# Performance work log

Hardware: AMD Instinct MI355X
Metric: run time of the kernel (lower is better)

Reference implementation:

```python
import jax, jax.numpy as jnp
import numpy as np

N, D_IN, D_OUT, E, TOPK = 2048, 2048, 2048, 8, 2


def setup_inputs() -> dict:
    key = jax.random.key(0)
    k1, k2, k3, k4 = jax.random.split(key, 4)
    inputs = jax.random.normal(k1, (N, D_IN), dtype=jnp.float32)
    weight = jax.random.normal(k2, (E, D_OUT, D_IN), dtype=jnp.float32) * (1.0 / np.sqrt(D_IN))
    gates = jax.random.uniform(k3, (N, TOPK), dtype=jnp.float32)
    gates = gates / jnp.sum(gates, axis=-1, keepdims=True)
    # random routing: expert id for each of the N*TOPK (token, slot) pairs
    expert_of = jax.random.randint(k4, (N * TOPK,), 0, E, dtype=jnp.int32)
    order = jnp.argsort(expert_of)  # positions sorted by expert id
    sorted_expert_idxs = expert_of[order].astype(jnp.int32)
    sorted_scattered_idxs = order.astype(jnp.int32)
    counts = jnp.bincount(expert_of, length=E)
    expert_offsets = jnp.cumsum(counts).astype(jnp.int32)
    padded_block_idxs = jnp.zeros((1,), dtype=jnp.int32)  # kernel blocking artifact, no math effect
    return {
        "inputs": inputs,
        "weight": weight,
        "k": TOPK,
        "sorted_expert_idxs": sorted_expert_idxs,
        "sorted_scattered_idxs": sorted_scattered_idxs,
        "padded_block_idxs": padded_block_idxs,
        "expert_offsets": expert_offsets,
        "gates": gates,
    }


def reference(inputs, weight, k, sorted_expert_idxs, sorted_scattered_idxs,
              padded_block_idxs, expert_offsets, gates):
    # inputs: [N, d_in]; weight: [E, d_out, d_in] (module permutes to [E, d_in, d_out])
    n_tok, d_in = inputs.shape
    n_e, d_out, _ = weight.shape
    nk = sorted_expert_idxs.shape[0]
    # invert the sort: expert id per flat (token, slot) position
    expert_of = jnp.zeros((nk,), dtype=sorted_expert_idxs.dtype).at[sorted_scattered_idxs].set(sorted_expert_idxs)
    x_flat = inputs[jnp.arange(nk) // k]  # [N*k, d_in] (fan-out of k per token)
    # grouped GEMM: y_flat[j] = x_flat[j] @ weight[expert_of[j]].T
    y_flat = jnp.zeros((nk, d_out), dtype=inputs.dtype)
    for e in range(n_e):  # loop over fixed small expert count (structural)
        mask = (expert_of == e)[:, None]
        y_flat = y_flat + jnp.where(mask, x_flat, 0.0) @ weight[e].T
    # gating combine: bmm(gates[:, None, :], y.view(N, k, d_out))
    out = jnp.einsum('nk,nkd->nd', gates, y_flat.reshape(n_tok, k, d_out))
    return out
```

## Files before the change

kernel.cpp:

```cpp
#include <hip/hip_runtime.h>
#include <hip/hip_bf16.h>

#define DIN   2048
#define DOUT  2048
#define NTOK  2048
#define NE    8
#define TOPK  2
#define NK    (NTOK*TOPK)
#define BM    256
#define BN    128
#define BK    32
#define KSPLIT 2
#define KLOC  (DIN/KSPLIT)
#define NKT   (KLOC/BK)
#define MAXMT (NK/BM + NE)
#define NTN   (DOUT/BN)
#define NBLK  (MAXMT*NTN*KSPLIT)

#define WEL (NE*DOUT*DIN)
#define XEL (NTOK*DIN)

typedef unsigned short u16;
typedef __attribute__((ext_vector_type(8))) short bf16x8;
typedef __attribute__((ext_vector_type(4))) float f32x4;

__device__ __forceinline__ unsigned pack2rn(float a, float b) {
    union { float f; unsigned u; } x, y; x.f = a; y.f = b;
    return __builtin_amdgcn_perm(y.u + 0x8000u, x.u + 0x8000u, 0x07060302u);
}

__device__ __forceinline__ void gl_lds16(const void* g, void* l) {
    __builtin_amdgcn_global_load_lds(
        (const __attribute__((address_space(1))) void*)g,
        (__attribute__((address_space(3)))       void*)l, 16, 0, 0);
}

__global__ __launch_bounds__(256) void cvt_x(
    const float* __restrict__ x, u16* __restrict__ xbf)
{
    const size_t nch = (size_t)XEL / 8;
    for (size_t c = (size_t)blockIdx.x * blockDim.x + threadIdx.x; c < nch;
         c += (size_t)gridDim.x * blockDim.x) {
        size_t off = c * 8;
        float4 f0 = *(const float4*)(x + off);
        float4 f1 = *(const float4*)(x + off + 4);
        uint4 pk;
        pk.x = pack2rn(f0.x, f0.y); pk.y = pack2rn(f0.z, f0.w);
        pk.z = pack2rn(f1.x, f1.y); pk.w = pack2rn(f1.z, f1.w);
        *(uint4*)(xbf + off) = pk;
    }
}

__global__ __launch_bounds__(512, 4) void moe_gemm_wf2(
    const u16*   __restrict__ xb,
    const float* __restrict__ wf,
    const int*   __restrict__ sorted_scattered_idxs,
    const int*   __restrict__ expert_offsets,
    const float* __restrict__ gates,
    float*       __restrict__ out)
{
    __shared__ u16 As[2][BM * BK];
    __shared__ u16 Bs[2][BN * BK];
    __shared__ int   s_tok[BM];
    __shared__ float s_gate[BM];

    const int bid = blockIdx.x;
    const int swz = (bid & 7) * (NBLK / 8) + (bid >> 3);
    const int n0  = (swz & (NTN - 1)) * BN;
    const int ksl = (swz >> 4) & (KSPLIT - 1);
    const int mt  = swz >> 5;

    int e = -1, m0 = 0, cnt = 0;
    {
        int acc0 = 0, prev = 0;
        for (int i = 0; i < NE; ++i) {
            int end = expert_offsets[i];
            int c = end - prev;
            int t = (c + BM - 1) / BM;
            if (mt < acc0 + t) {
                e = i; m0 = prev + (mt - acc0) * BM;
                cnt = end - m0; if (cnt > BM) cnt = BM;
                break;
            }
            acc0 += t; prev = end;
        }
    }
    if (e < 0) return;

    const int tid = threadIdx.x;
    if (tid < BM) {
        int idx = (tid < cnt) ? (m0 + tid) : m0;
        int p = sorted_scattered_idxs[idx];
        s_tok[tid]  = p;
        s_gate[tid] = gates[p];
    }
    __syncthreads();

    const int wid = tid >> 6, lane = tid & 63;
    const int kbase = ksl * KLOC;

    const int arow0 = wid * 16 + (lane >> 2);
    const int cga   = (lane & 3) ^ ((lane >> 3) & 3);
    const u16* aS0 = xb + (size_t)(s_tok[arow0] >> 1) * DIN + kbase + cga * 8;
    const u16* aS1 = xb + (size_t)(s_tok[arow0 + 128] >> 1) * DIN + kbase + cga * 8;
    const int adst0 = (wid * 16) * BK;
    const int adst1 = (128 + wid * 16) * BK;

    const int brow = tid >> 2;
    const int bch  = tid & 3;
    const int bcg  = bch ^ ((brow >> 1) & 3);
    const float* bF = wf + (size_t)e * DOUT * DIN + (size_t)(n0 + brow) * DIN + kbase + bch * 8;
    const int bwr = brow * BK + bcg * 8;

    const int wr = wid >> 2, wc = wid & 3;
    const int lr = lane & 15, g = lane >> 4;
    const int xch = (g ^ ((lr >> 1) & 3)) * 8;
    int aoff[8], boff[2];
    #pragma unroll
    for (int mi = 0; mi < 8; ++mi) aoff[mi] = (wr * 128 + mi * 16 + lr) * BK + xch;
    #pragma unroll
    for (int n = 0; n < 2; ++n)    boff[n]  = (wc * 32 + n * 16 + lr) * BK + xch;

    f32x4 acc[8][2];
    #pragma unroll
    for (int mi = 0; mi < 8; ++mi)
        #pragma unroll
        for (int n = 0; n < 2; ++n) acc[mi][n] = (f32x4)0.0f;

    float4 pb0, pb1;

#define STGA(buf, t)                                                          \
    {                                                                         \
        const int ko = (t) * BK;                                              \
        gl_lds16(aS0 + ko, &As[buf][adst0]);                                  \
        gl_lds16(aS1 + ko, &As[buf][adst1]);                                  \
    }

#define BGLB(t)                                                               \
    {                                                                         \
        const int ko = (t) * BK;                                              \
        pb0 = *(const float4*)(bF + ko);                                      \
        pb1 = *(const float4*)(bF + ko + 4);                                  \
    }

#define BPACK(buf)                                                            \
    {                                                                         \
        uint4 w;                                                              \
        w.x = pack2rn(pb0.x, pb0.y); w.y = pack2rn(pb0.z, pb0.w);             \
        w.z = pack2rn(pb1.x, pb1.y); w.w = pack2rn(pb1.z, pb1.w);             \
        *(uint4*)(&Bs[buf][bwr]) = w;                                         \
    }

#define BODY(b)                                                               \
    {                                                                         \
        bf16x8 bfv[2], af[4], ag[4];                                          \
        bfv[0] = *(const bf16x8*)(&Bs[b][boff[0]]);                           \
        bfv[1] = *(const bf16x8*)(&Bs[b][boff[1]]);                           \
        _Pragma("unroll")                                                     \
        for (int mi = 0; mi < 4; ++mi)                                        \
            af[mi] = *(const bf16x8*)(&As[b][aoff[mi]]);                      \
        __builtin_amdgcn_s_setprio(1);                                        \
        _Pragma("unroll")                                                     \
        for (int mi = 0; mi < 4; ++mi) {                                      \
            acc[mi][0] = __builtin_amdgcn_mfma_f32_16x16x32_bf16(             \
                af[mi], bfv[0], acc[mi][0], 0, 0, 0);                         \
            acc[mi][1] = __builtin_amdgcn_mfma_f32_16x16x32_bf16(             \
                af[mi], bfv[1], acc[mi][1], 0, 0, 0);                         \
        }                                                                     \
        _Pragma("unroll")                                                     \
        for (int mi = 0; mi < 4; ++mi)                                        \
            ag[mi] = *(const bf16x8*)(&As[b][aoff[mi + 4]]);                  \
        _Pragma("unroll")                                                     \
        for (int mi = 0; mi < 4; ++mi) {                                      \
            acc[mi+4][0] = __builtin_amdgcn_mfma_f32_16x16x32_bf16(           \
                ag[mi], bfv[0], acc[mi+4][0], 0, 0, 0);                       \
            acc[mi+4][1] = __builtin_amdgcn_mfma_f32_16x16x32_bf16(           \
                ag[mi], bfv[1], acc[mi+4][1], 0, 0, 0);                       \
        }                                                                     \
        __builtin_amdgcn_s_setprio(0);                                        \
        __builtin_amdgcn_s_barrier();                                        \
    }

    BGLB(0);
    STGA(0, 0);
    asm volatile("s_waitcnt vmcnt(0)" ::: "memory");
    __builtin_amdgcn_sched_barrier(0);
    BPACK(0);
    STGA(1, 1);
    BGLB(1);

    #pragma unroll 2
    for (int t = 0; t < NKT; ++t) {
        asm volatile("s_waitcnt lgkmcnt(0)" ::: "memory");
        __builtin_amdgcn_s_barrier();
        BODY(t & 1);
        asm volatile("s_waitcnt vmcnt(0)" ::: "memory");
        __builtin_amdgcn_sched_barrier(0);
        if (t + 1 < NKT) BPACK((t + 1) & 1);
        if (t + 2 < NKT) { STGA(t & 1, t + 2); BGLB(t + 2); }
    }

#undef STGA
#undef BGLB
#undef BPACK
#undef BODY

    #pragma unroll
    for (int mi = 0; mi < 8; ++mi) {
        #pragma unroll
        for (int r = 0; r < 4; ++r) {
            int lrow = wr * 128 + mi * 16 + g * 4 + r;
            if (lrow < cnt) {
                int   p  = s_tok[lrow];
                float gf = s_gate[lrow];
                float* orow = out + (size_t)(p >> 1) * DOUT + n0 + wc * 32;
                #pragma unroll
                for (int n = 0; n < 2; ++n)
                    atomicAdd(orow + n * 16 + lr, gf * acc[mi][n][r]);
            }
        }
    }
}

#define FBM 128
#define FBK 64
__global__ __launch_bounds__(256, 3) void moe_gemm_fused(
    const float* __restrict__ inputs, const float* __restrict__ weight,
    const int* __restrict__ sorted_scattered_idxs, const int* __restrict__ expert_offsets,
    const float* __restrict__ gates, float* __restrict__ out)
{
    __shared__ u16 As[FBM * FBK];
    __shared__ u16 Bs[FBM * FBK];
    __shared__ int   s_tok[FBM];
    __shared__ float s_gate[FBM];

    const int mt = blockIdx.y;
    const int n0 = blockIdx.x * FBM;
    int e = -1, m0 = 0, cnt = 0;
    {
        int acc = 0, prev = 0;
        for (int i = 0; i < NE; ++i) {
            int end = expert_offsets[i];
            int c = end - prev;
            int t = (c + FBM - 1) / FBM;
            if (mt < acc + t) {
                e = i; m0 = prev + (mt - acc) * FBM;
                cnt = end - m0; if (cnt > FBM) cnt = FBM;
                break;
            }
            acc += t; prev = end;
        }
    }
    if (e < 0) return;

    const int tid = threadIdx.x;
    if (tid < FBM) {
        int idx = (tid < cnt) ? (m0 + tid) : m0;
        int p = sorted_scattered_idxs[idx];
        s_tok[tid]  = p;
        s_gate[tid] = gates[p];
    }
    __syncthreads();

    const int ch  = tid & 7;
    const int r0  = tid >> 3;
    const int sch = ch ^ (r0 & 7);
    const float* wbase = weight + (size_t)e * DOUT * DIN;
    const float* ap[4]; const float* bp[4];
    #pragma unroll
    for (int i = 0; i < 4; ++i) {
        int r = r0 + 32 * i;
        ap[i] = inputs + (size_t)(s_tok[r] >> 1) * DIN + ch * 8;
        bp[i] = wbase + (size_t)(n0 + r) * DIN + ch * 8;
    }
    u16* aw = &As[r0 * FBK + sch * 8];
    u16* bw = &Bs[r0 * FBK + sch * 8];

    const int wid = tid >> 6, lane = tid & 63;
    const int wm = (wid >> 1) * 64, wn = (wid & 1) * 64;
    const int g  = lane >> 4, lr = lane & 15;

    f32x4 acc[4][4];
    #pragma unroll
    for (int i = 0; i < 4; ++i)
        #pragma unroll
        for (int j = 0; j < 4; ++j) acc[i][j] = (f32x4)0.0f;

    float4 pa[4][2], pb[4][2];
    #pragma unroll
    for (int i = 0; i < 4; ++i) {
        pa[i][0] = *(const float4*)(ap[i] + 0); pa[i][1] = *(const float4*)(ap[i] + 4);
        pb[i][0] = *(const float4*)(bp[i] + 0); pb[i][1] = *(const float4*)(bp[i] + 4);
    }
    for (int kt = 0; kt < DIN / FBK; ++kt) {
        __syncthreads();
        #pragma unroll
        for (int i = 0; i < 4; ++i) {
            uint4 va, vb;
            va.x = pack2rn(pa[i][0].x, pa[i][0].y); va.y = pack2rn(pa[i][0].z, pa[i][0].w);
            va.z = pack2rn(pa[i][1].x, pa[i][1].y); va.w = pack2rn(pa[i][1].z, pa[i][1].w);
            *(uint4*)(aw + i * 32 * FBK) = va;
            vb.x = pack2rn(pb[i][0].x, pb[i][0].y); vb.y = pack2rn(pb[i][0].z, pb[i][0].w);
            vb.z = pack2rn(pb[i][1].x, pb[i][1].y); vb.w = pack2rn(pb[i][1].z, pb[i][1].w);
            *(uint4*)(bw + i * 32 * FBK) = vb;
        }
        __syncthreads();
        if (kt + 1 < DIN / FBK) {
            const int kof = (kt + 1) * FBK;
            #pragma unroll
            for (int i = 0; i < 4; ++i) {
                pa[i][0] = *(const float4*)(ap[i] + kof); pa[i][1] = *(const float4*)(ap[i] + kof + 4);
                pb[i][0] = *(const float4*)(bp[i] + kof); pb[i][1] = *(const float4*)(bp[i] + kof + 4);
            }
        }
        #pragma unroll
        for (int ks = 0; ks < 2; ++ks) {
            bf16x8 a[4], b[4];
            #pragma unroll
            for (int i = 0; i < 4; ++i) {
                int ra = wm + i * 16 + lr; int ca = (ks * 4 + g) ^ (ra & 7);
                a[i] = *(const bf16x8*)(&As[ra * FBK + ca * 8]);
                int rb = wn + i * 16 + lr; int cb = (ks * 4 + g) ^ (rb & 7);
                b[i] = *(const bf16x8*)(&Bs[rb * FBK + cb * 8]);
            }
            #pragma unroll
            for (int i = 0; i < 4; ++i)
                #pragma unroll
                for (int j = 0; j < 4; ++j)
                    acc[i][j] = __builtin_amdgcn_mfma_f32_16x16x32_bf16(a[i], b[j], acc[i][j], 0, 0, 0);
        }
    }
    #pragma unroll
    for (int i = 0; i < 4; ++i) {
        #pragma unroll
        for (int j2 = 0; j2 < 4; ++j2) {
            int lrow = wm + i * 16 + g * 4 + j2;
            if (lrow < cnt) {
                int   p  = s_tok[lrow];
                float gf = s_gate[lrow];
                float* orow = out + (size_t)(p >> 1) * DOUT + n0 + wn;
                #pragma unroll
                for (int nf = 0; nf < 4; ++nf)
                    atomicAdd(orow + nf * 16 + lr, gf * acc[i][nf][j2]);
            }
        }
    }
}

extern "C" void kernel_launch(void* const* d_in, const int* in_sizes, int n_in,
                              void* d_out, int out_size, void* d_ws, size_t ws_size,
                              hipStream_t stream) {
    const float* inputs  = (const float*)d_in[0];
    const float* weight  = (const float*)d_in[1];
    const int*   ssi     = (const int*)d_in[4];
    const int*   eoff    = (const int*)d_in[6];
    const float* gates   = (const float*)d_in[7];
    float* out = (float*)d_out;

    hipMemsetAsync(out, 0, (size_t)out_size * sizeof(float), stream);

    const size_t need = (size_t)XEL * sizeof(u16);
    if (ws_size >= need) {
        u16* xbf = (u16*)d_ws;
        cvt_x<<<1024, 256, 0, stream>>>(inputs, xbf);
        moe_gemm_wf2<<<NBLK, 512, 0, stream>>>(xbf, weight, ssi, eoff, gates, out);
    } else {
        dim3 grid(DOUT / FBM, NK / FBM + NE);
        moe_gemm_fused<<<grid, 256, 0, stream>>>(inputs, weight, ssi, eoff, gates, out);
    }
}
```

Baseline: 113.1 us.

## Pre-convert weights to bf16 and stream both operands via direct-to-LDS loads

Expands the conversion kernel to also turn the fp32 expert weights into bf16 in the workspace. The GEMM then loads both A and B tiles with global_load_lds, dropping the register staging and in-loop packing of fp32 weights, and uses a vmcnt-counted double-buffered pipeline. In exchange, every call pays an extra full pass that reads the fp32 weights and writes a bf16 copy, and the workspace requirement grows to hold that copy.

```diff
diff --git a/kernel.cpp b/kernel.cpp
--- a/kernel.cpp
+++ b/kernel.cpp
@@ -35,29 +35,32 @@
         (__attribute__((address_space(3)))       void*)l, 16, 0, 0);
 }
 
-__global__ __launch_bounds__(256) void cvt_x(
-    const float* __restrict__ x, u16* __restrict__ xbf)
+__global__ __launch_bounds__(256) void cvt_bf16(
+    const float* __restrict__ w, const float* __restrict__ x,
+    u16* __restrict__ wbf, u16* __restrict__ xbf)
 {
-    const size_t nch = (size_t)XEL / 8;
+    const size_t nch = (size_t)(WEL + XEL) / 8;
     for (size_t c = (size_t)blockIdx.x * blockDim.x + threadIdx.x; c < nch;
          c += (size_t)gridDim.x * blockDim.x) {
-        size_t off = c * 8;
-        float4 f0 = *(const float4*)(x + off);
-        float4 f1 = *(const float4*)(x + off + 4);
+        const float* src; u16* dst; size_t off;
+        if (c < (size_t)WEL / 8) { src = w; dst = wbf; off = c * 8; }
+        else                     { src = x; dst = xbf; off = (c - (size_t)WEL / 8) * 8; }
+        float4 f0 = *(const float4*)(src + off);
+        float4 f1 = *(const float4*)(src + off + 4);
         uint4 pk;
         pk.x = pack2rn(f0.x, f0.y); pk.y = pack2rn(f0.z, f0.w);
         pk.z = pack2rn(f1.x, f1.y); pk.w = pack2rn(f1.z, f1.w);
-        *(uint4*)(xbf + off) = pk;
-    }
-}
-
-__global__ __launch_bounds__(512, 4) void moe_gemm_wf2(
-    const u16*   __restrict__ xb,
-    const float* __restrict__ wf,
-    const int*   __restrict__ sorted_scattered_idxs,
-    const int*   __restrict__ expert_offsets,
+        *(uint4*)(dst + off) = pk;
+    }
+}
+
+__global__ __launch_bounds__(512, 4) void moe_bf3(
+    const u16* __restrict__ xb,
+    const u16* __restrict__ wb,
+    const int* __restrict__ sorted_scattered_idxs,
+    const int* __restrict__ expert_offsets,
     const float* __restrict__ gates,
-    float*       __restrict__ out)
+    float*     __restrict__ out)
 {
     __shared__ u16 As[2][BM * BK];
     __shared__ u16 Bs[2][BN * BK];
@@ -107,10 +110,9 @@
     const int adst1 = (128 + wid * 16) * BK;
 
     const int brow = tid >> 2;
-    const int bch  = tid & 3;
-    const int bcg  = bch ^ ((brow >> 1) & 3);
-    const float* bF = wf + (size_t)e * DOUT * DIN + (size_t)(n0 + brow) * DIN + kbase + bch * 8;
-    const int bwr = brow * BK + bcg * 8;
+    const int bcg  = (tid & 3) ^ ((brow >> 1) & 3);
+    const u16* bS = wb + (size_t)e * DOUT * DIN + (size_t)(n0 + brow) * DIN + kbase + bcg * 8;
+    const int bdst = (wid * 16) * BK;
 
     const int wr = wid >> 2, wc = wid & 3;
     const int lr = lane & 15, g = lane >> 4;
@@ -127,28 +129,12 @@
         #pragma unroll
         for (int n = 0; n < 2; ++n) acc[mi][n] = (f32x4)0.0f;
 
-    float4 pb0, pb1;
-
-#define STGA(buf, t)                                                          \
+#define STG(buf, t)                                                           \
     {                                                                         \
         const int ko = (t) * BK;                                              \
         gl_lds16(aS0 + ko, &As[buf][adst0]);                                  \
         gl_lds16(aS1 + ko, &As[buf][adst1]);                                  \
-    }
-
-#define BGLB(t)                                                               \
-    {                                                                         \
-        const int ko = (t) * BK;                                              \
-        pb0 = *(const float4*)(bF + ko);                                      \
-        pb1 = *(const float4*)(bF + ko + 4);                                  \
-    }
-
-#define BPACK(buf)                                                            \
-    {                                                                         \
-        uint4 w;                                                              \
-        w.x = pack2rn(pb0.x, pb0.y); w.y = pack2rn(pb0.z, pb0.w);             \
-        w.z = pack2rn(pb1.x, pb1.y); w.w = pack2rn(pb1.z, pb1.w);             \
-        *(uint4*)(&Bs[buf][bwr]) = w;                                         \
+        gl_lds16(bS  + ko, &Bs[buf][bdst]);                                   \
     }
 
 #define BODY(b)                                                               \
@@ -181,28 +167,30 @@
         __builtin_amdgcn_s_barrier();                                        \
     }
 
-    BGLB(0);
-    STGA(0, 0);
-    asm volatile("s_waitcnt vmcnt(0)" ::: "memory");
-    __builtin_amdgcn_sched_barrier(0);
-    BPACK(0);
-    STGA(1, 1);
-    BGLB(1);
-
-    #pragma unroll 2
-    for (int t = 0; t < NKT; ++t) {
-        asm volatile("s_waitcnt lgkmcnt(0)" ::: "memory");
+    STG(0, 0);
+    STG(1, 1);
+
+    for (int t = 0; t < NKT - 2; ++t) {
+        asm volatile("s_waitcnt vmcnt(3)" ::: "memory");
+        __builtin_amdgcn_sched_barrier(0);
         __builtin_amdgcn_s_barrier();
         BODY(t & 1);
+        STG(t & 1, t + 2);
+    }
+    {
+        asm volatile("s_waitcnt vmcnt(3)" ::: "memory");
+        __builtin_amdgcn_sched_barrier(0);
+        __builtin_amdgcn_s_barrier();
+        BODY((NKT - 2) & 1);
+    }
+    {
         asm volatile("s_waitcnt vmcnt(0)" ::: "memory");
         __builtin_amdgcn_sched_barrier(0);
-        if (t + 1 < NKT) BPACK((t + 1) & 1);
-        if (t + 2 < NKT) { STGA(t & 1, t + 2); BGLB(t + 2); }
-    }
-
-#undef STGA
-#undef BGLB
-#undef BPACK
+        __builtin_amdgcn_s_barrier();
+        BODY((NKT - 1) & 1);
+    }
+
+#undef STG
 #undef BODY
 
     #pragma unroll
@@ -359,11 +347,12 @@
 
     hipMemsetAsync(out, 0, (size_t)out_size * sizeof(float), stream);
 
-    const size_t need = (size_t)XEL * sizeof(u16);
+    const size_t need = ((size_t)WEL + (size_t)XEL) * sizeof(u16);
     if (ws_size >= need) {
-        u16* xbf = (u16*)d_ws;
-        cvt_x<<<1024, 256, 0, stream>>>(inputs, xbf);
-        moe_gemm_wf2<<<NBLK, 512, 0, stream>>>(xbf, weight, ssi, eoff, gates, out);
+        u16* wbf = (u16*)d_ws;
+        u16* xbf = wbf + (size_t)WEL;
+        cvt_bf16<<<2048, 256, 0, stream>>>(weight, inputs, wbf, xbf);
+        moe_bf3<<<NBLK, 512, 0, stream>>>(xbf, wbf, ssi, eoff, gates, out);
     } else {
         dim3 grid(DOUT / FBM, NK / FBM + NE);
         moe_gemm_fused<<<grid, 256, 0, stream>>>(inputs, weight, ssi, eoff, gates, out);
```

Result: slower. 138.1 us (+22.1%).

## Keep two B-tile global loads in flight with partial vmcnt waits instead of draining

Applied to the files above, without the earlier changes.

The K-loop is restructured so the fp32 weight loads for the next two tiles are held in two separate register sets. Each iteration now waits with vmcnt(4) instead of vmcnt(0), so the prefetch two steps ahead stays outstanding while the current tile is packed and computed. This targets stalls from fully draining the memory queue every iteration. The launch-bounds occupancy hint drops from 4 to 2 blocks per SM to leave room for the extra prefetch registers, which can reduce waves per CU.

```diff
diff --git a/kernel.cpp b/kernel.cpp
--- a/kernel.cpp
+++ b/kernel.cpp
@@ -51,7 +51,7 @@
     }
 }
 
-__global__ __launch_bounds__(512, 4) void moe_gemm_wf2(
+__global__ __launch_bounds__(512, 2) void moe_nodrain(
     const u16*   __restrict__ xb,
     const float* __restrict__ wf,
     const int*   __restrict__ sorted_scattered_idxs,
@@ -127,7 +127,7 @@
         #pragma unroll
         for (int n = 0; n < 2; ++n) acc[mi][n] = (f32x4)0.0f;
 
-    float4 pb0, pb1;
+    float4 pbA0, pbA1, pbB0, pbB1;
 
 #define STGA(buf, t)                                                          \
     {                                                                         \
@@ -136,18 +136,18 @@
         gl_lds16(aS1 + ko, &As[buf][adst1]);                                  \
     }
 
-#define BGLB(t)                                                               \
+#define BGLB(t, P0, P1)                                                       \
     {                                                                         \
         const int ko = (t) * BK;                                              \
-        pb0 = *(const float4*)(bF + ko);                                      \
-        pb1 = *(const float4*)(bF + ko + 4);                                  \
-    }
-
-#define BPACK(buf)                                                            \
+        P0 = *(const float4*)(bF + ko);                                       \
+        P1 = *(const float4*)(bF + ko + 4);                                   \
+    }
+
+#define BPACK(buf, P0, P1)                                                    \
     {                                                                         \
         uint4 w;                                                              \
-        w.x = pack2rn(pb0.x, pb0.y); w.y = pack2rn(pb0.z, pb0.w);             \
-        w.z = pack2rn(pb1.x, pb1.y); w.w = pack2rn(pb1.z, pb1.w);             \
+        w.x = pack2rn(P0.x, P0.y); w.y = pack2rn(P0.z, P0.w);                 \
+        w.z = pack2rn(P1.x, P1.y); w.w = pack2rn(P1.z, P1.w);                 \
         *(uint4*)(&Bs[buf][bwr]) = w;                                         \
     }
 
@@ -178,32 +178,37 @@
                 ag[mi], bfv[1], acc[mi+4][1], 0, 0, 0);                       \
         }                                                                     \
         __builtin_amdgcn_s_setprio(0);                                        \
-        __builtin_amdgcn_s_barrier();                                        \
-    }
-
-    BGLB(0);
-    STGA(0, 0);
-    asm volatile("s_waitcnt vmcnt(0)" ::: "memory");
-    __builtin_amdgcn_sched_barrier(0);
-    BPACK(0);
-    STGA(1, 1);
-    BGLB(1);
-
-    #pragma unroll 2
-    for (int t = 0; t < NKT; ++t) {
-        asm volatile("s_waitcnt lgkmcnt(0)" ::: "memory");
-        __builtin_amdgcn_s_barrier();
-        BODY(t & 1);
-        asm volatile("s_waitcnt vmcnt(0)" ::: "memory");
-        __builtin_amdgcn_sched_barrier(0);
-        if (t + 1 < NKT) BPACK((t + 1) & 1);
-        if (t + 2 < NKT) { STGA(t & 1, t + 2); BGLB(t + 2); }
-    }
+        __builtin_amdgcn_s_barrier();                                         \
+        __builtin_amdgcn_sched_barrier(0);                                    \
+    }
+
+#define ITER(t, P0, P1, VW)                                                   \
+    {                                                                         \
+        asm volatile("s_waitcnt vmcnt(" #VW ")" ::: "memory");                \
+        __builtin_amdgcn_sched_barrier(0);                                    \
+        BPACK((t) & 1, P0, P1);                                               \
+        asm volatile("s_waitcnt lgkmcnt(0)" ::: "memory");                    \
+        __builtin_amdgcn_s_barrier();                                         \
+        __builtin_amdgcn_sched_barrier(0);                                    \
+        BODY((t) & 1);                                                        \
+        if ((t) + 2 < NKT) { STGA((t) & 1, (t) + 2); BGLB((t) + 2, P0, P1); } \
+    }
+
+    STGA(0, 0); BGLB(0, pbA0, pbA1);
+    STGA(1, 1); BGLB(1, pbB0, pbB1);
+
+    for (int tt = 0; tt < NKT - 2; tt += 2) {
+        ITER(tt,     pbA0, pbA1, 4)
+        ITER(tt + 1, pbB0, pbB1, 4)
+    }
+    ITER(NKT - 2, pbA0, pbA1, 4)
+    ITER(NKT - 1, pbB0, pbB1, 0)
 
 #undef STGA
 #undef BGLB
 #undef BPACK
 #undef BODY
+#undef ITER
 
     #pragma unroll
     for (int mi = 0; mi < 8; ++mi) {
@@ -363,7 +368,7 @@
     if (ws_size >= need) {
         u16* xbf = (u16*)d_ws;
         cvt_x<<<1024, 256, 0, stream>>>(inputs, xbf);
-        moe_gemm_wf2<<<NBLK, 512, 0, stream>>>(xbf, weight, ssi, eoff, gates, out);
+        moe_nodrain<<<NBLK, 512, 0, stream>>>(xbf, weight, ssi, eoff, gates, out);
     } else {
         dim3 grid(DOUT / FBM, NK / FBM + NE);
         moe_gemm_fused<<<grid, 256, 0, stream>>>(inputs, weight, ssi, eoff, gates, out);
```

After: 115.7 us. +2.3%, slower.
